# Kernel tuning notes

Measured on AMD Instinct MI355X. Metric: run time of the kernel, lower is better.

The kernel has to match this reference:

```python
import jax, jax.numpy as jnp
import numpy as np

N_ATOMS = 25000
N_PAIRS = 500000
C = 64        # pp_nodes[-1] == ii_nodes[-1]
PI_N = 32     # pi_nodes[-1]
NB = 8        # n_basis
N_PROPS = 2   # rank//2 + 1 for rank=3


def setup_inputs() -> dict:
    key = jax.random.key(0)
    ks = jax.random.split(key, 16)
    g = lambda k, s, fan: (jax.random.normal(k, s, jnp.float32) / np.float32(np.sqrt(fan)))
    ind_2 = jax.random.randint(ks[0], (N_PAIRS, 2), 0, N_ATOMS, dtype=jnp.int32)
    p1 = jax.random.normal(ks[1], (N_ATOMS, C), jnp.float32)
    p3 = jax.random.normal(ks[2], (N_ATOMS, 3, C), jnp.float32)
    d3 = jax.random.normal(ks[3], (N_PAIRS, 3), jnp.float32)
    basis = jax.random.normal(ks[4], (N_PAIRS, NB), jnp.float32)
    # InvarLayer params
    W_pi = g(ks[5], (2 * C, PI_N * NB), 2 * C)   # PILayer FF (bias, tanh)
    b_pi = jnp.zeros((PI_N * NB,), jnp.float32)
    W_ii = g(ks[6], (PI_N, C * N_PROPS), PI_N)   # ii layer, no bias
    W_pp = g(ks[7], (C * N_PROPS, C), 2 * C)     # pp layer, no bias
    # EquiVarLayer (rank 3) params
    wi_pix = g(ks[8], (C, C), C)
    wj_pix = g(ks[9], (C, C), C)
    W_ppx = g(ks[10], (C, C), C)                 # pp layer: no bias, no activation
    wi_dot = g(ks[11], (C, C), C)
    wj_dot = g(ks[12], (C, C), C)
    # GCBlock final pp layer (bias, tanh)
    W_pp1 = g(ks[13], (2 * C, 2 * C), 2 * C)
    b_pp1 = jnp.zeros((2 * C,), jnp.float32)
    return dict(ind_2=ind_2, p1=p1, p3=p3, d3=d3, basis=basis,
                W_pi=W_pi, b_pi=b_pi, W_ii=W_ii, W_pp=W_pp,
                wi_pix=wi_pix, wj_pix=wj_pix, W_ppx=W_ppx,
                wi_dot=wi_dot, wj_dot=wj_dot, W_pp1=W_pp1, b_pp1=b_pp1)


def reference(ind_2, p1, p3, d3, basis, W_pi, b_pi, W_ii, W_pp,
              wi_pix, wj_pix, W_ppx, wi_dot, wj_dot, W_pp1, b_pp1):
    ii = ind_2[:, 0]
    jj = ind_2[:, 1]
    n_atoms = p1.shape[0]

    # ---- InvarLayer ----
    # PILayer: gather pair endpoints, FF to [P, PI_N*NB], contract with basis
    inter = jnp.concatenate([p1[ii], p1[jj]], axis=-1)         # [P, 2C]
    inter = jnp.tanh(inter @ W_pi + b_pi)                      # [P, PI_N*NB]
    inter = inter.reshape(-1, PI_N, NB)
    i1_pre = jnp.einsum('pcb,pb->pc', inter, basis)            # [P, PI_N]
    # ii FF (no bias)
    i1 = jnp.tanh(i1_pre @ W_ii)                               # [P, 2C]
    # IPLayer: scatter-sum interactions to atoms
    p1_agg = jax.ops.segment_sum(i1, ii, num_segments=n_atoms) # [N, 2C]
    p1_new = jnp.tanh(p1_agg @ W_pp)                           # [N, C]

    i1_0, i1_1 = jnp.split(i1, N_PROPS, axis=-1)               # each [P, C]

    # ---- EquiVarLayer (rank 3) ----
    # weighted PIXLayer: channel-mix gathered endpoint vectors
    ix = (jnp.einsum('pxc,cd->pxd', p3[ii], wi_pix)
          + jnp.einsum('pxc,cd->pxd', p3[jj], wj_pix))         # [P, 3, C]
    # scale(ix, i1) + scale(diff[:, :, None], i1)
    ix = (ix + d3[:, :, None]) * i1_1[:, None, :]              # [P, 3, C]
    p3_agg = jax.ops.segment_sum(ix, ii, num_segments=n_atoms) # [N, 3, C]
    p3_mixed = jnp.einsum('nxc,cd->nxd', p3_agg, W_ppx)        # [N, 3, C]
    # weighted DotLayer: reduce the equivariant axis
    dotted_p3 = jnp.einsum('nxr,nxr->nr',
                           jnp.einsum('nxc,cr->nxr', p3_mixed, wi_dot),
                           jnp.einsum('nxc,cr->nxr', p3_mixed, wj_dot))  # [N, C]

    # ---- GCBlock stitch ----
    p1t1 = jnp.tanh(jnp.concatenate([p1_new, dotted_p3], axis=-1) @ W_pp1 + b_pp1)  # [N, 2C]
    p1_out, s3 = jnp.split(p1t1, N_PROPS, axis=-1)             # each [N, C]
    p3_out = p3_mixed * s3[:, None, :]                         # [N, 3, C]
    return (p1_out, p3_out, dotted_p3, i1, ix)
```

## Files before the change

### kernel.cpp

```cpp
#include <hip/hip_runtime.h>

#define NP 500000
#define NA 25000

__device__ __forceinline__ float tanh_fast(float x) {
    float e = __expf(2.0f * x);
    return 1.0f - 2.0f / (e + 1.0f);
}

__device__ __forceinline__ float readlane_f(float v, int lane) {
    int iv = __builtin_bit_cast(int, v);
    int r = __builtin_amdgcn_readlane(iv, lane);
    return __builtin_bit_cast(float, r);
}

__device__ __forceinline__ float dpp8_reduce(float s) {
    int x;
    x = __builtin_amdgcn_update_dpp(0, __builtin_bit_cast(int, s), 0xB1, 0xF, 0xF, true);
    s += __builtin_bit_cast(float, x);
    x = __builtin_amdgcn_update_dpp(0, __builtin_bit_cast(int, s), 0x4E, 0xF, 0xF, true);
    s += __builtin_bit_cast(float, x);
    x = __builtin_amdgcn_update_dpp(0, __builtin_bit_cast(int, s), 0x141, 0xF, 0xF, true);
    s += __builtin_bit_cast(float, x);
    return s;
}

__device__ __forceinline__ unsigned short f2bf(float x) {
    union { float f; unsigned int u; } c; c.f = x;
    unsigned int r = c.u + 0x7FFFu + ((c.u >> 16) & 1u);
    return (unsigned short)(r >> 16);
}
__device__ __forceinline__ float bf2f(unsigned short h) {
    union { unsigned int u; float f; } c; c.u = ((unsigned int)h) << 16;
    return c.f;
}
__device__ __forceinline__ unsigned int pack2bf(float a, float b) {
    return (unsigned int)f2bf(a) | ((unsigned int)f2bf(b) << 16);
}
__device__ __forceinline__ float lo_bf(unsigned int x) { return bf2f((unsigned short)(x & 0xffffu)); }
__device__ __forceinline__ float hi_bf(unsigned int x) { return bf2f((unsigned short)(x >> 16)); }
__device__ __forceinline__ float lo_bf_f(unsigned int x) {
    return __builtin_bit_cast(float, x << 16);
}
__device__ __forceinline__ float hi_bf_f(unsigned int x) {
    return __builtin_bit_cast(float, x & 0xffff0000u);
}

extern "C" __global__ __launch_bounds__(256, 2)
void k0_uv(const float* __restrict__ p1,
           const float* __restrict__ W_pi,
           const float* __restrict__ b_pi,
           float* __restrict__ u,
           unsigned short* __restrict__ vq)
{
    __shared__ float sW[32 * 256];
    __shared__ float sp1[16 * 64];

    const int t = threadIdx.x;
    const int wv = t >> 6;
    const int l = t & 63;
    const int atom0 = blockIdx.x * 16;

    #pragma unroll
    for (int f = 0; f < 4; ++f) {
        int idx = f * 256 + t;
        int at = atom0 + (idx >> 6);
        int atc = at < NA ? at : NA - 1;
        sp1[idx] = p1[(size_t)atc * 64 + (idx & 63)];
    }

    float accu[4][4] = {{0}}, accv[4][4] = {{0}};

    #pragma unroll
    for (int s = 0; s < 4; ++s) {
        __syncthreads();
        {
            const float4* src = (const float4*)(W_pi + s * 32 * 256);
            float4* dst = (float4*)sW;
            #pragma unroll
            for (int f = 0; f < 8; ++f) dst[f * 256 + t] = src[f * 256 + t];
        }
        __syncthreads();
        const int kbase = (s & 1) * 32;
        #pragma unroll 2
        for (int k = 0; k < 32; ++k) {
            float wq[4];
            #pragma unroll
            for (int q = 0; q < 4; ++q) wq[q] = sW[k * 256 + 64 * q + l];
            #pragma unroll
            for (int a = 0; a < 4; ++a) {
                float pv = sp1[(wv * 4 + a) * 64 + kbase + k];
                #pragma unroll
                for (int q = 0; q < 4; ++q) {
                    if (s < 2) accu[a][q] = fmaf(pv, wq[q], accu[a][q]);
                    else       accv[a][q] = fmaf(pv, wq[q], accv[a][q]);
                }
            }
        }
    }

    #pragma unroll
    for (int a = 0; a < 4; ++a) {
        const int at = atom0 + wv * 4 + a;
        if (at < NA) {
            #pragma unroll
            for (int q = 0; q < 4; ++q)
                u[(size_t)at * 256 + 64 * q + l] = accu[a][q] + b_pi[64 * q + l];
            uint2 vv;
            vv.x = pack2bf(accv[a][0], accv[a][1]);
            vv.y = pack2bf(accv[a][2], accv[a][3]);
            *(uint2*)&vq[(size_t)at * 512 + 8 * l] = vv;
        }
    }
}

extern "C" __global__ __launch_bounds__(256, 4)
void k0_q(const float* __restrict__ p3,
          const float* __restrict__ wi_pix,
          const float* __restrict__ wj_pix,
          const int* __restrict__ ind2,
          int* __restrict__ cnt,
          unsigned short* __restrict__ qi_bf,
          unsigned short* __restrict__ vq)
{
    __shared__ float sWi[64 * 64];
    __shared__ float sWj[64 * 64];

    const int t = threadIdx.x;

    {
        int gp = blockIdx.x * 256 + t;
        if (gp < NP) atomicAdd(&cnt[ind2[2 * gp]], 1);
    }

    {
        const float4* si = (const float4*)wi_pix;
        const float4* sj = (const float4*)wj_pix;
        float4* di = (float4*)sWi;
        float4* dj = (float4*)sWj;
        #pragma unroll
        for (int f = 0; f < 4; ++f) { di[f * 256 + t] = si[f * 256 + t]; dj[f * 256 + t] = sj[f * 256 + t]; }
    }
    __syncthreads();

    const int w = t >> 6;
    const int l = t & 63;
    const int atom = blockIdx.x * 4 + w;

    float val0 = p3[((size_t)atom * 3 + 0) * 64 + l];
    float val1 = p3[((size_t)atom * 3 + 1) * 64 + l];
    float val2 = p3[((size_t)atom * 3 + 2) * 64 + l];

    float ai[3] = {0, 0, 0}, aj[3] = {0, 0, 0};
    #pragma unroll 8
    for (int k = 0; k < 64; ++k) {
        float a0 = readlane_f(val0, k);
        float a1 = readlane_f(val1, k);
        float a2 = readlane_f(val2, k);
        float wi = sWi[k * 64 + l];
        float wj = sWj[k * 64 + l];
        ai[0] = fmaf(a0, wi, ai[0]); aj[0] = fmaf(a0, wj, aj[0]);
        ai[1] = fmaf(a1, wi, ai[1]); aj[1] = fmaf(a1, wj, aj[1]);
        ai[2] = fmaf(a2, wi, ai[2]); aj[2] = fmaf(a2, wj, aj[2]);
    }
    uint2 iu, ju;
    iu.x = pack2bf(ai[0], ai[1]); iu.y = pack2bf(ai[2], 0.0f);
    ju.x = pack2bf(aj[0], aj[1]); ju.y = pack2bf(aj[2], 0.0f);
    *(uint2*)&qi_bf[(size_t)atom * 256 + 4 * l] = iu;
    *(uint2*)&vq[(size_t)atom * 512 + 8 * l + 4] = ju;
}

extern "C" __global__ __launch_bounds__(1024)
void csr_scan(const int* __restrict__ cnt, int* __restrict__ rowstart)
{
    __shared__ int ssum[1024];
    const int t = threadIdx.x;
    const int base = t * 25;

    int s = 0;
    #pragma unroll 5
    for (int i = 0; i < 25; ++i) {
        int idx = base + i;
        s += (idx < NA) ? cnt[idx] : 0;
    }
    ssum[t] = s;
    __syncthreads();
    for (int off = 1; off < 1024; off <<= 1) {
        int vv = (t >= off) ? ssum[t - off] : 0;
        __syncthreads();
        ssum[t] += vv;
        __syncthreads();
    }
    int run = (t > 0) ? ssum[t - 1] : 0;
    for (int i = 0; i < 25; ++i) {
        int idx = base + i;
        if (idx <= NA) rowstart[idx] = run;
        run += (idx < NA) ? cnt[idx] : 0;
    }
}

extern "C" __global__ void k_scatter(const int* __restrict__ ind2,
                                     const int* __restrict__ rowstart,
                                     int* __restrict__ cursor,
                                     int2* __restrict__ plist2)
{
    int p = blockIdx.x * 256 + threadIdx.x;
    if (p < NP) {
        int ii = ind2[2 * p];
        int jj = ind2[2 * p + 1];
        int pos = atomicAdd(&cursor[ii], 1);
        plist2[rowstart[ii] + pos] = make_int2(p, jj);
    }
}

extern "C" __global__ __launch_bounds__(256, 4)
void k_pair(const float* __restrict__ d3,
            const float* __restrict__ basis,
            const float* __restrict__ W_ii,
            const float* __restrict__ u,
            const unsigned short* __restrict__ vq,
            const unsigned short* __restrict__ qi_bf,
            const int* __restrict__ rowstart,
            const int2* __restrict__ plist2,
            float* __restrict__ out_i1,
            float* __restrict__ out_ix,
            float* __restrict__ p1_agg,
            float* __restrict__ p3_agg)
{
    const int t = threadIdx.x;
    const int w = t >> 6;
    const int l = t & 63;
    const int n = blockIdx.x * 4 + w;

    unsigned int wAB[32];
    #pragma unroll
    for (int c = 0; c < 32; ++c)
        wAB[c] = pack2bf(W_ii[c * 128 + l], W_ii[c * 128 + 64 + l]);

    float uu[4];
    #pragma unroll
    for (int q = 0; q < 4; ++q) uu[q] = u[(size_t)n * 256 + 64 * q + l];
    float qiv[3];
    {
        uint2 iu = *(const uint2*)&qi_bf[(size_t)n * 256 + 4 * l];
        qiv[0] = lo_bf(iu.x); qiv[1] = hi_bf(iu.x); qiv[2] = lo_bf(iu.y);
    }

    const int start = rowstart[n];
    const int end   = rowstart[n + 1];

    float agg1a = 0.0f, agg1b = 0.0f;
    float agg30 = 0.0f, agg31 = 0.0f, agg32 = 0.0f;

    if (start < end) {
        const int last = end - 1;

        int2 pj0, pj1;
        uint4 vq0, vq1;
        float bs0, bs1;
        float d0x, d0y, d0z, d1x, d1y, d1z;

        {
            int iA = start;
            int iB = (start + 1 <= last) ? start + 1 : last;
            pj0 = plist2[iA];
            pj1 = plist2[iB];
            vq0 = *(const uint4*)&vq[(size_t)pj0.y * 512 + 8 * l];
            vq1 = *(const uint4*)&vq[(size_t)pj1.y * 512 + 8 * l];
            bs0 = basis[(size_t)pj0.x * 8 + (l & 7)];
            bs1 = basis[(size_t)pj1.x * 8 + (l & 7)];
            d0x = d3[3 * (size_t)pj0.x + 0]; d0y = d3[3 * (size_t)pj0.x + 1]; d0z = d3[3 * (size_t)pj0.x + 2];
            d1x = d3[3 * (size_t)pj1.x + 0]; d1y = d3[3 * (size_t)pj1.x + 1]; d1z = d3[3 * (size_t)pj1.x + 2];
        }

        for (int it = start; it < end; it += 2) {
            int iC = (it + 2 <= last) ? it + 2 : last;
            int iD = (it + 3 <= last) ? it + 3 : last;
            int2 pjT0 = plist2[iC];
            int2 pjT1 = plist2[iD];
            uint4 vqT0 = *(const uint4*)&vq[(size_t)pjT0.y * 512 + 8 * l];
            uint4 vqT1 = *(const uint4*)&vq[(size_t)pjT1.y * 512 + 8 * l];
            float bsT0 = basis[(size_t)pjT0.x * 8 + (l & 7)];
            float bsT1 = basis[(size_t)pjT1.x * 8 + (l & 7)];
            float dT0x = d3[3 * (size_t)pjT0.x + 0];
            float dT0y = d3[3 * (size_t)pjT0.x + 1];
            float dT0z = d3[3 * (size_t)pjT0.x + 2];
            float dT1x = d3[3 * (size_t)pjT1.x + 0];
            float dT1y = d3[3 * (size_t)pjT1.x + 1];
            float dT1z = d3[3 * (size_t)pjT1.x + 2];

            float h00 = tanh_fast(uu[0] + lo_bf(vq0.x));
            float h10 = tanh_fast(uu[0] + lo_bf(vq1.x));
            float h01 = tanh_fast(uu[1] + hi_bf(vq0.x));
            float h11 = tanh_fast(uu[1] + hi_bf(vq1.x));
            float h02 = tanh_fast(uu[2] + lo_bf(vq0.y));
            float h12 = tanh_fast(uu[2] + lo_bf(vq1.y));
            float h03 = tanh_fast(uu[3] + hi_bf(vq0.y));
            float h13 = tanh_fast(uu[3] + hi_bf(vq1.y));

            float pre0[4], pre1[4];
            pre0[0] = dpp8_reduce(h00 * bs0);
            pre1[0] = dpp8_reduce(h10 * bs1);
            pre0[1] = dpp8_reduce(h01 * bs0);
            pre1[1] = dpp8_reduce(h11 * bs1);
            pre0[2] = dpp8_reduce(h02 * bs0);
            pre1[2] = dpp8_reduce(h12 * bs1);
            pre0[3] = dpp8_reduce(h03 * bs0);
            pre1[3] = dpp8_reduce(h13 * bs1);

            float a0A = 0, a0B = 0, a1A = 0, a1B = 0;
            float b0A = 0, b0B = 0, b1A = 0, b1B = 0;
            #pragma unroll
            for (int c = 0; c < 32; c += 2) {
                float p00 = readlane_f(pre0[c >> 3], 8 * (c & 7));
                float p10 = readlane_f(pre1[c >> 3], 8 * (c & 7));
                float p01 = readlane_f(pre0[(c + 1) >> 3], 8 * ((c + 1) & 7));
                float p11 = readlane_f(pre1[(c + 1) >> 3], 8 * ((c + 1) & 7));
                float wlo0 = lo_bf_f(wAB[c]), whi0 = hi_bf_f(wAB[c]);
                float wlo1 = lo_bf_f(wAB[c + 1]), whi1 = hi_bf_f(wAB[c + 1]);
                a0A = fmaf(p00, wlo0, a0A);  b0A = fmaf(p00, whi0, b0A);
                a1A = fmaf(p10, wlo0, a1A);  b1A = fmaf(p10, whi0, b1A);
                a0B = fmaf(p01, wlo1, a0B);  b0B = fmaf(p01, whi1, b0B);
                a1B = fmaf(p11, wlo1, a1B);  b1B = fmaf(p11, whi1, b1B);
            }
            const float i10_0 = tanh_fast(a0A + a0B);
            const float i11_0 = tanh_fast(b0A + b0B);
            const float i10_1 = tanh_fast(a1A + a1B);
            const float i11_1 = tanh_fast(b1A + b1B);

            {
                const size_t pA = (size_t)pj0.x;
                __builtin_nontemporal_store(i10_0, &out_i1[pA * 128 + l]);
                __builtin_nontemporal_store(i11_0, &out_i1[pA * 128 + 64 + l]);
                agg1a += i10_0;
                agg1b += i11_0;
                float ix0 = (qiv[0] + lo_bf(vq0.z) + d0x) * i11_0;
                float ix1 = (qiv[1] + hi_bf(vq0.z) + d0y) * i11_0;
                float ix2 = (qiv[2] + lo_bf(vq0.w) + d0z) * i11_0;
                __builtin_nontemporal_store(ix0, &out_ix[(pA * 3 + 0) * 64 + l]);
                __builtin_nontemporal_store(ix1, &out_ix[(pA * 3 + 1) * 64 + l]);
                __builtin_nontemporal_store(ix2, &out_ix[(pA * 3 + 2) * 64 + l]);
                agg30 += ix0; agg31 += ix1; agg32 += ix2;
            }
            if (it + 1 < end) {
                const size_t pA = (size_t)pj1.x;
                __builtin_nontemporal_store(i10_1, &out_i1[pA * 128 + l]);
                __builtin_nontemporal_store(i11_1, &out_i1[pA * 128 + 64 + l]);
                agg1a += i10_1;
                agg1b += i11_1;
                float ix0 = (qiv[0] + lo_bf(vq1.z) + d1x) * i11_1;
                float ix1 = (qiv[1] + hi_bf(vq1.z) + d1y) * i11_1;
                float ix2 = (qiv[2] + lo_bf(vq1.w) + d1z) * i11_1;
                __builtin_nontemporal_store(ix0, &out_ix[(pA * 3 + 0) * 64 + l]);
                __builtin_nontemporal_store(ix1, &out_ix[(pA * 3 + 1) * 64 + l]);
                __builtin_nontemporal_store(ix2, &out_ix[(pA * 3 + 2) * 64 + l]);
                agg30 += ix0; agg31 += ix1; agg32 += ix2;
            }

            pj0 = pjT0; vq0 = vqT0; bs0 = bsT0; d0x = dT0x; d0y = dT0y; d0z = dT0z;
            pj1 = pjT1; vq1 = vqT1; bs1 = bsT1; d1x = dT1x; d1y = dT1y; d1z = dT1z;
        }
    }

    p1_agg[(size_t)n * 128 + l]      = agg1a;
    p1_agg[(size_t)n * 128 + 64 + l] = agg1b;
    p3_agg[(size_t)n * 192 + l]       = agg30;
    p3_agg[(size_t)n * 192 + 64 + l]  = agg31;
    p3_agg[(size_t)n * 192 + 128 + l] = agg32;
}

extern "C" __global__ __launch_bounds__(256, 4)
void k3_atoms(const float* __restrict__ p1_agg,
              const float* __restrict__ p3_agg,
              const float* __restrict__ W_pp,
              const float* __restrict__ W_ppx,
              const float* __restrict__ wi_dot,
              const float* __restrict__ wj_dot,
              const float* __restrict__ W_pp1,
              const float* __restrict__ b_pp1,
              float* __restrict__ out_p1,
              float* __restrict__ out_p3,
              float* __restrict__ out_dot)
{
    __shared__ float s1[4][128];
    __shared__ float s3[4][192];
    __shared__ float sPm[4][192];
    __shared__ float sCat[4][128];

    const int w = threadIdx.x >> 6;
    const int l = threadIdx.x & 63;
    const int n = blockIdx.x * 4 + w;

    s1[w][l]      = p1_agg[(size_t)n * 128 + l];
    s1[w][64 + l] = p1_agg[(size_t)n * 128 + 64 + l];
    #pragma unroll
    for (int x = 0; x < 3; ++x)
        s3[w][x * 64 + l] = p3_agg[(size_t)n * 192 + x * 64 + l];
    __syncthreads();

    float pn = 0.0f;
    #pragma unroll 4
    for (int k = 0; k < 128; ++k)
        pn = fmaf(s1[w][k], W_pp[k * 64 + l], pn);
    pn = tanh_fast(pn);

    float pm[3];
    #pragma unroll
    for (int x = 0; x < 3; ++x) {
        float s = 0.0f;
        #pragma unroll 4
        for (int c = 0; c < 64; ++c)
            s = fmaf(s3[w][x * 64 + c], W_ppx[c * 64 + l], s);
        pm[x] = s;
        sPm[w][x * 64 + l] = s;
    }
    __syncthreads();

    float dot = 0.0f;
    #pragma unroll
    for (int x = 0; x < 3; ++x) {
        float vi = 0.0f, vj = 0.0f;
        #pragma unroll 4
        for (int c = 0; c < 64; ++c) {
            float a = sPm[w][x * 64 + c];
            vi = fmaf(a, wi_dot[c * 64 + l], vi);
            vj = fmaf(a, wj_dot[c * 64 + l], vj);
        }
        dot = fmaf(vi, vj, dot);
    }

    sCat[w][l]      = pn;
    sCat[w][64 + l] = dot;
    __syncthreads();

    float u1 = b_pp1[l];
    float u2 = b_pp1[64 + l];
    #pragma unroll 4
    for (int k = 0; k < 128; ++k) {
        float ck = sCat[w][k];
        u1 = fmaf(ck, W_pp1[k * 128 + l], u1);
        u2 = fmaf(ck, W_pp1[k * 128 + 64 + l], u2);
    }
    float p1o = tanh_fast(u1);
    float s3v = tanh_fast(u2);

    out_p1[(size_t)n * 64 + l]  = p1o;
    out_dot[(size_t)n * 64 + l] = dot;
    #pragma unroll
    for (int x = 0; x < 3; ++x)
        out_p3[((size_t)n * 3 + x) * 64 + l] = pm[x] * s3v;
}

extern "C" void kernel_launch(void* const* d_in, const int* in_sizes, int n_in,
                              void* d_out, int out_size, void* d_ws, size_t ws_size,
                              hipStream_t stream)
{
    const int*   ind2   = (const int*)d_in[0];
    const float* p1     = (const float*)d_in[1];
    const float* p3     = (const float*)d_in[2];
    const float* d3     = (const float*)d_in[3];
    const float* basis  = (const float*)d_in[4];
    const float* W_pi   = (const float*)d_in[5];
    const float* b_pi   = (const float*)d_in[6];
    const float* W_ii   = (const float*)d_in[7];
    const float* W_pp   = (const float*)d_in[8];
    const float* wi_pix = (const float*)d_in[9];
    const float* wj_pix = (const float*)d_in[10];
    const float* W_ppx  = (const float*)d_in[11];
    const float* wi_dot = (const float*)d_in[12];
    const float* wj_dot = (const float*)d_in[13];
    const float* W_pp1  = (const float*)d_in[14];
    const float* b_pp1  = (const float*)d_in[15];

    float* out     = (float*)d_out;
    float* out_p1  = out;
    float* out_p3  = out + 1600000;
    float* out_dot = out + 6400000;
    float* out_i1  = out + 8000000;
    float* out_ix  = out + 72000000;

    float*          u      = (float*)d_ws;
    unsigned short* vq     = (unsigned short*)(u + 6400000);
    unsigned short* qi_bf  = vq + 12800000;
    float*          p1_agg = (float*)(qi_bf + 6400000);
    float*          p3_agg = p1_agg + 3200000;
    int2*           plist2 = (int2*)(p3_agg + 4800000);
    int*            cnt      = (int*)(plist2 + 500000);
    int*            rowstart = cnt + 25000;
    int*            cursor   = rowstart + 25001;

    hipMemsetAsync(cnt, 0, (size_t)75001 * sizeof(int), stream);

    dim3 blk(256);
    k0_uv    <<<dim3(1563), blk, 0, stream>>>(p1, W_pi, b_pi, u, vq);
    k0_q     <<<dim3(6250), blk, 0, stream>>>(p3, wi_pix, wj_pix, ind2, cnt,
                                              qi_bf, vq);
    csr_scan <<<dim3(1), dim3(1024), 0, stream>>>(cnt, rowstart);
    k_scatter<<<dim3(1954), blk, 0, stream>>>(ind2, rowstart, cursor, plist2);
    k_pair   <<<dim3(6250), blk, 0, stream>>>(d3, basis, W_ii, u, vq,
                                              qi_bf, rowstart, plist2,
                                              out_i1, out_ix, p1_agg, p3_agg);
    k3_atoms <<<dim3(6250), blk, 0, stream>>>(p1_agg, p3_agg, W_pp, W_ppx,
                                              wi_dot, wj_dot, W_pp1, b_pp1,
                                              out_p1, out_p3, out_dot);
}
```

Baseline: 590.3 us.

## Pack per-pair d3/basis into CSR-ordered records and deepen prefetch pipeline

The scatter kernel now writes a 64-byte record per pair, holding the pair index, jj, d3 and basis, in CSR order. The pair kernel therefore streams contiguous records instead of doing dependent random gathers into d3 and basis through the pair index. The pair kernel's software pipeline goes from one stage to two: records are fetched two iterations ahead and vq rows one iteration ahead. tanh also switches to a fast divide. The trade-off is an extra 32 MB workspace write and read, plus more live registers in the pair loop.

```diff
diff --git a/kernel.cpp b/kernel.cpp
--- a/kernel.cpp
+++ b/kernel.cpp
@@ -5,7 +5,7 @@
 
 __device__ __forceinline__ float tanh_fast(float x) {
     float e = __expf(2.0f * x);
-    return 1.0f - 2.0f / (e + 1.0f);
+    return 1.0f - __fdividef(2.0f, e + 1.0f);
 }
 
 __device__ __forceinline__ float readlane_f(float v, int lane) {
@@ -200,28 +200,46 @@
 }
 
 extern "C" __global__ void k_scatter(const int* __restrict__ ind2,
+                                     const float* __restrict__ d3,
+                                     const float* __restrict__ basis,
                                      const int* __restrict__ rowstart,
                                      int* __restrict__ cursor,
-                                     int2* __restrict__ plist2)
+                                     float* __restrict__ prec)
 {
     int p = blockIdx.x * 256 + threadIdx.x;
     if (p < NP) {
         int ii = ind2[2 * p];
         int jj = ind2[2 * p + 1];
         int pos = atomicAdd(&cursor[ii], 1);
-        plist2[rowstart[ii] + pos] = make_int2(p, jj);
+        float* r = prec + (size_t)(rowstart[ii] + pos) * 16;
+        float4 b0 = *(const float4*)&basis[(size_t)p * 8];
+        float4 b1 = *(const float4*)&basis[(size_t)p * 8 + 4];
+        float4 r0;
+        r0.x = __builtin_bit_cast(float, p);
+        r0.y = __builtin_bit_cast(float, jj);
+        r0.z = d3[3 * (size_t)p + 0];
+        r0.w = d3[3 * (size_t)p + 1];
+        float4 r1;
+        r1.x = d3[3 * (size_t)p + 2];
+        r1.y = b0.x; r1.z = b0.y; r1.w = b0.z;
+        float4 r2;
+        r2.x = b0.w; r2.y = b1.x; r2.z = b1.y; r2.w = b1.z;
+        float4 r3;
+        r3.x = b1.w; r3.y = 0; r3.z = 0; r3.w = 0;
+        *(float4*)&r[0]  = r0;
+        *(float4*)&r[4]  = r1;
+        *(float4*)&r[8]  = r2;
+        *(float4*)&r[12] = r3;
     }
 }
 
 extern "C" __global__ __launch_bounds__(256, 4)
-void k_pair(const float* __restrict__ d3,
-            const float* __restrict__ basis,
+void k_pair(const float* __restrict__ prec,
             const float* __restrict__ W_ii,
             const float* __restrict__ u,
             const unsigned short* __restrict__ vq,
             const unsigned short* __restrict__ qi_bf,
             const int* __restrict__ rowstart,
-            const int2* __restrict__ plist2,
             float* __restrict__ out_i1,
             float* __restrict__ out_ix,
             float* __restrict__ p1_agg,
@@ -231,6 +249,7 @@
     const int w = t >> 6;
     const int l = t & 63;
     const int n = blockIdx.x * 4 + w;
+    const int lb = l & 7;
 
     unsigned int wAB[32];
     #pragma unroll
@@ -254,59 +273,79 @@
 
     if (start < end) {
         const int last = end - 1;
-
-        int2 pj0, pj1;
-        uint4 vq0, vq1;
-        float bs0, bs1;
-        float d0x, d0y, d0z, d1x, d1y, d1z;
+        auto clampi = [&](int i) { return i <= last ? i : last; };
+
+        int   Up0, Up1;
+        float Ud0x, Ud0y, Ud0z, Ud1x, Ud1y, Ud1z;
+        float Ubs0, Ubs1;
+        uint4 Uvq0, Uvq1;
+        int   Mp0, Mp1, Mj0, Mj1;
+        float Md0x, Md0y, Md0z, Md1x, Md1y, Md1z;
+        float Mbs0, Mbs1;
+        uint4 Mvq0, Mvq1;
 
         {
-            int iA = start;
-            int iB = (start + 1 <= last) ? start + 1 : last;
-            pj0 = plist2[iA];
-            pj1 = plist2[iB];
-            vq0 = *(const uint4*)&vq[(size_t)pj0.y * 512 + 8 * l];
-            vq1 = *(const uint4*)&vq[(size_t)pj1.y * 512 + 8 * l];
-            bs0 = basis[(size_t)pj0.x * 8 + (l & 7)];
-            bs1 = basis[(size_t)pj1.x * 8 + (l & 7)];
-            d0x = d3[3 * (size_t)pj0.x + 0]; d0y = d3[3 * (size_t)pj0.x + 1]; d0z = d3[3 * (size_t)pj0.x + 2];
-            d1x = d3[3 * (size_t)pj1.x + 0]; d1y = d3[3 * (size_t)pj1.x + 1]; d1z = d3[3 * (size_t)pj1.x + 2];
+            const float4* r0 = (const float4*)&prec[(size_t)clampi(start) * 16];
+            const float4* r1 = (const float4*)&prec[(size_t)clampi(start + 1) * 16];
+            float4 a0 = r0[0], a1 = r1[0];
+            Up0 = __builtin_bit_cast(int, a0.x);
+            int Uj0 = __builtin_bit_cast(int, a0.y);
+            Ud0x = a0.z; Ud0y = a0.w;
+            Ud0z = ((const float*)r0)[4];
+            Ubs0 = ((const float*)r0)[5 + lb];
+            Up1 = __builtin_bit_cast(int, a1.x);
+            int Uj1 = __builtin_bit_cast(int, a1.y);
+            Ud1x = a1.z; Ud1y = a1.w;
+            Ud1z = ((const float*)r1)[4];
+            Ubs1 = ((const float*)r1)[5 + lb];
+            Uvq0 = *(const uint4*)&vq[(size_t)Uj0 * 512 + 8 * l];
+            Uvq1 = *(const uint4*)&vq[(size_t)Uj1 * 512 + 8 * l];
+
+            const float4* m0 = (const float4*)&prec[(size_t)clampi(start + 2) * 16];
+            const float4* m1 = (const float4*)&prec[(size_t)clampi(start + 3) * 16];
+            float4 b0 = m0[0], b1 = m1[0];
+            Mp0 = __builtin_bit_cast(int, b0.x);
+            Mj0 = __builtin_bit_cast(int, b0.y);
+            Md0x = b0.z; Md0y = b0.w;
+            Md0z = ((const float*)m0)[4];
+            Mbs0 = ((const float*)m0)[5 + lb];
+            Mp1 = __builtin_bit_cast(int, b1.x);
+            Mj1 = __builtin_bit_cast(int, b1.y);
+            Md1x = b1.z; Md1y = b1.w;
+            Md1z = ((const float*)m1)[4];
+            Mbs1 = ((const float*)m1)[5 + lb];
+            Mvq0 = *(const uint4*)&vq[(size_t)Mj0 * 512 + 8 * l];
+            Mvq1 = *(const uint4*)&vq[(size_t)Mj1 * 512 + 8 * l];
         }
 
         for (int it = start; it < end; it += 2) {
-            int iC = (it + 2 <= last) ? it + 2 : last;
-            int iD = (it + 3 <= last) ? it + 3 : last;
-            int2 pjT0 = plist2[iC];
-            int2 pjT1 = plist2[iD];
-            uint4 vqT0 = *(const uint4*)&vq[(size_t)pjT0.y * 512 + 8 * l];
-            uint4 vqT1 = *(const uint4*)&vq[(size_t)pjT1.y * 512 + 8 * l];
-            float bsT0 = basis[(size_t)pjT0.x * 8 + (l & 7)];
-            float bsT1 = basis[(size_t)pjT1.x * 8 + (l & 7)];
-            float dT0x = d3[3 * (size_t)pjT0.x + 0];
-            float dT0y = d3[3 * (size_t)pjT0.x + 1];
-            float dT0z = d3[3 * (size_t)pjT0.x + 2];
-            float dT1x = d3[3 * (size_t)pjT1.x + 0];
-            float dT1y = d3[3 * (size_t)pjT1.x + 1];
-            float dT1z = d3[3 * (size_t)pjT1.x + 2];
-
-            float h00 = tanh_fast(uu[0] + lo_bf(vq0.x));
-            float h10 = tanh_fast(uu[0] + lo_bf(vq1.x));
-            float h01 = tanh_fast(uu[1] + hi_bf(vq0.x));
-            float h11 = tanh_fast(uu[1] + hi_bf(vq1.x));
-            float h02 = tanh_fast(uu[2] + lo_bf(vq0.y));
-            float h12 = tanh_fast(uu[2] + lo_bf(vq1.y));
-            float h03 = tanh_fast(uu[3] + hi_bf(vq0.y));
-            float h13 = tanh_fast(uu[3] + hi_bf(vq1.y));
+            const float4* r0 = (const float4*)&prec[(size_t)clampi(it + 4) * 16];
+            const float4* r1 = (const float4*)&prec[(size_t)clampi(it + 5) * 16];
+            float4 ra = r0[0];
+            float  rz0 = ((const float*)r0)[4];
+            float  rb0 = ((const float*)r0)[5 + lb];
+            float4 rb = r1[0];
+            float  rz1 = ((const float*)r1)[4];
+            float  rb1 = ((const float*)r1)[5 + lb];
+
+            float h00 = tanh_fast(uu[0] + lo_bf(Uvq0.x));
+            float h10 = tanh_fast(uu[0] + lo_bf(Uvq1.x));
+            float h01 = tanh_fast(uu[1] + hi_bf(Uvq0.x));
+            float h11 = tanh_fast(uu[1] + hi_bf(Uvq1.x));
+            float h02 = tanh_fast(uu[2] + lo_bf(Uvq0.y));
+            float h12 = tanh_fast(uu[2] + lo_bf(Uvq1.y));
+            float h03 = tanh_fast(uu[3] + hi_bf(Uvq0.y));
+            float h13 = tanh_fast(uu[3] + hi_bf(Uvq1.y));
 
             float pre0[4], pre1[4];
-            pre0[0] = dpp8_reduce(h00 * bs0);
-            pre1[0] = dpp8_reduce(h10 * bs1);
-            pre0[1] = dpp8_reduce(h01 * bs0);
-            pre1[1] = dpp8_reduce(h11 * bs1);
-            pre0[2] = dpp8_reduce(h02 * bs0);
-            pre1[2] = dpp8_reduce(h12 * bs1);
-            pre0[3] = dpp8_reduce(h03 * bs0);
-            pre1[3] = dpp8_reduce(h13 * bs1);
+            pre0[0] = dpp8_reduce(h00 * Ubs0);
+            pre1[0] = dpp8_reduce(h10 * Ubs1);
+            pre0[1] = dpp8_reduce(h01 * Ubs0);
+            pre1[1] = dpp8_reduce(h11 * Ubs1);
+            pre0[2] = dpp8_reduce(h02 * Ubs0);
+            pre1[2] = dpp8_reduce(h12 * Ubs1);
+            pre0[3] = dpp8_reduce(h03 * Ubs0);
+            pre1[3] = dpp8_reduce(h13 * Ubs1);
 
             float a0A = 0, a0B = 0, a1A = 0, a1B = 0;
             float b0A = 0, b0B = 0, b1A = 0, b1B = 0;
@@ -329,36 +368,48 @@
             const float i11_1 = tanh_fast(b1A + b1B);
 
             {
-                const size_t pA = (size_t)pj0.x;
+                const size_t pA = (size_t)Up0;
                 __builtin_nontemporal_store(i10_0, &out_i1[pA * 128 + l]);
                 __builtin_nontemporal_store(i11_0, &out_i1[pA * 128 + 64 + l]);
                 agg1a += i10_0;
                 agg1b += i11_0;
-                float ix0 = (qiv[0] + lo_bf(vq0.z) + d0x) * i11_0;
-                float ix1 = (qiv[1] + hi_bf(vq0.z) + d0y) * i11_0;
-                float ix2 = (qiv[2] + lo_bf(vq0.w) + d0z) * i11_0;
+                float ix0 = (qiv[0] + lo_bf(Uvq0.z) + Ud0x) * i11_0;
+                float ix1 = (qiv[1] + hi_bf(Uvq0.z) + Ud0y) * i11_0;
+                float ix2 = (qiv[2] + lo_bf(Uvq0.w) + Ud0z) * i11_0;
                 __builtin_nontemporal_store(ix0, &out_ix[(pA * 3 + 0) * 64 + l]);
                 __builtin_nontemporal_store(ix1, &out_ix[(pA * 3 + 1) * 64 + l]);
                 __builtin_nontemporal_store(ix2, &out_ix[(pA * 3 + 2) * 64 + l]);
                 agg30 += ix0; agg31 += ix1; agg32 += ix2;
             }
             if (it + 1 < end) {
-                const size_t pA = (size_t)pj1.x;
+                const size_t pA = (size_t)Up1;
                 __builtin_nontemporal_store(i10_1, &out_i1[pA * 128 + l]);
                 __builtin_nontemporal_store(i11_1, &out_i1[pA * 128 + 64 + l]);
                 agg1a += i10_1;
                 agg1b += i11_1;
-                float ix0 = (qiv[0] + lo_bf(vq1.z) + d1x) * i11_1;
-                float ix1 = (qiv[1] + hi_bf(vq1.z) + d1y) * i11_1;
-                float ix2 = (qiv[2] + lo_bf(vq1.w) + d1z) * i11_1;
+                float ix0 = (qiv[0] + lo_bf(Uvq1.z) + Ud1x) * i11_1;
+                float ix1 = (qiv[1] + hi_bf(Uvq1.z) + Ud1y) * i11_1;
+                float ix2 = (qiv[2] + lo_bf(Uvq1.w) + Ud1z) * i11_1;
                 __builtin_nontemporal_store(ix0, &out_ix[(pA * 3 + 0) * 64 + l]);
                 __builtin_nontemporal_store(ix1, &out_ix[(pA * 3 + 1) * 64 + l]);
                 __builtin_nontemporal_store(ix2, &out_ix[(pA * 3 + 2) * 64 + l]);
                 agg30 += ix0; agg31 += ix1; agg32 += ix2;
             }
 
-            pj0 = pjT0; vq0 = vqT0; bs0 = bsT0; d0x = dT0x; d0y = dT0y; d0z = dT0z;
-            pj1 = pjT1; vq1 = vqT1; bs1 = bsT1; d1x = dT1x; d1y = dT1y; d1z = dT1z;
+            Up0 = Mp0; Up1 = Mp1;
+            Ud0x = Md0x; Ud0y = Md0y; Ud0z = Md0z;
+            Ud1x = Md1x; Ud1y = Md1y; Ud1z = Md1z;
+            Ubs0 = Mbs0; Ubs1 = Mbs1;
+            Uvq0 = Mvq0; Uvq1 = Mvq1;
+
+            Mp0 = __builtin_bit_cast(int, ra.x);
+            Mj0 = __builtin_bit_cast(int, ra.y);
+            Md0x = ra.z; Md0y = ra.w; Md0z = rz0; Mbs0 = rb0;
+            Mp1 = __builtin_bit_cast(int, rb.x);
+            Mj1 = __builtin_bit_cast(int, rb.y);
+            Md1x = rb.z; Md1y = rb.w; Md1z = rz1; Mbs1 = rb1;
+            Mvq0 = *(const uint4*)&vq[(size_t)Mj0 * 512 + 8 * l];
+            Mvq1 = *(const uint4*)&vq[(size_t)Mj1 * 512 + 8 * l];
         }
     }
 
@@ -484,8 +535,8 @@
     unsigned short* qi_bf  = vq + 12800000;
     float*          p1_agg = (float*)(qi_bf + 6400000);
     float*          p3_agg = p1_agg + 3200000;
-    int2*           plist2 = (int2*)(p3_agg + 4800000);
-    int*            cnt      = (int*)(plist2 + 500000);
+    float*          prec   = p3_agg + 4800000;
+    int*            cnt      = (int*)(prec + 8000000 + 32);
     int*            rowstart = cnt + 25000;
     int*            cursor   = rowstart + 25001;
 
@@ -496,9 +547,9 @@
     k0_q     <<<dim3(6250), blk, 0, stream>>>(p3, wi_pix, wj_pix, ind2, cnt,
                                               qi_bf, vq);
     csr_scan <<<dim3(1), dim3(1024), 0, stream>>>(cnt, rowstart);
-    k_scatter<<<dim3(1954), blk, 0, stream>>>(ind2, rowstart, cursor, plist2);
-    k_pair   <<<dim3(6250), blk, 0, stream>>>(d3, basis, W_ii, u, vq,
-                                              qi_bf, rowstart, plist2,
+    k_scatter<<<dim3(1954), blk, 0, stream>>>(ind2, d3, basis, rowstart, cursor, prec);
+    k_pair   <<<dim3(6250), blk, 0, stream>>>(prec, W_ii, u, vq,
+                                              qi_bf, rowstart,
                                               out_i1, out_ix, p1_agg, p3_agg);
     k3_atoms <<<dim3(6250), blk, 0, stream>>>(p1_agg, p3_agg, W_pp, W_ppx,
                                               wi_dot, wj_dot, W_pp1, b_pp1,
```

New measurement: 752.6 us. 27.5% more time.
